# Optimization experiments

Hardware: AMD Instinct MI355X
Metric: run time of the kernel (lower is better)

## Reference

```python
import jax, jax.numpy as jnp
import numpy as np

FP4_E2M1_VALUES = [0.0, 0.0625, 8.0, 1.0, 2.0, 3.0, 4.0, 6.0,
                   -0.0, -0.0625, -8.0, -1.0, -2.0, -3.0, -4.0, -6.0]

M, N, K = 4096, 4096, 4096


def setup_inputs() -> dict:
    key = jax.random.key(0)
    k1, k2 = jax.random.split(key)
    x = jax.random.normal(k1, (M, K), dtype=jnp.float16)
    # packed uint8 bytes stored as int32 (values in [0,256)); each byte holds
    # two fp4 indices: high nibble = even k, low nibble = odd k
    packed_weight = jax.random.randint(k2, (N, K // 2), 0, 256, dtype=jnp.int32)
    lut = jnp.array(FP4_E2M1_VALUES, dtype=jnp.float16)
    return {"x": x, "packed_weight": packed_weight, "lut": lut}


def reference(x, packed_weight, lut):
    # Dequantize: unpack nibbles along K, LUT lookup -> W [N, K] fp16
    n, kh = packed_weight.shape
    high = (packed_weight >> 4) & 15   # even k positions
    low = packed_weight & 15           # odd k positions
    idx = jnp.stack([high, low], axis=-1).reshape(n, 2 * kh)  # [N, K]
    w = lut[idx]                       # [N, K] fp16
    # GEMM with fp32 accumulation (Triton kernel accumulates in fp32), cast to fp16
    y = jnp.einsum('mk,nk->mn', x, w, preferred_element_type=jnp.float32)
    return y.astype(jnp.float16)
```

## Files before the change

### kernel.cpp

```cpp
#include <hip/hip_runtime.h>
#include <hip/hip_fp16.h>
#include <stdint.h>

#define M_DIM 4096
#define N_DIM 4096
#define K_DIM 4096
#define BM 128
#define BN 128
#define BK 32
#define KW (K_DIM / 2)

typedef _Float16 half8 __attribute__((ext_vector_type(8)));
typedef float f32x4 __attribute__((ext_vector_type(4)));

__device__ __forceinline__ uint32_t pk2(float a, float b) {
  auto h = __builtin_amdgcn_cvt_pkrtz(a, b);
  return __builtin_bit_cast(uint32_t, h);
}

__device__ __forceinline__ uint32_t dq(uint32_t b, uint32_t ph, uint32_t pl) {
#if __has_builtin(__builtin_amdgcn_perm)
  const uint32_t sel = ((b & 0x70u) << 4) | ((b & 0x07u) << 24);
  uint32_t v = __builtin_amdgcn_perm(ph, pl, sel);
#else
  const uint64_t pool = ((uint64_t)ph << 32) | pl;
  const uint32_t mh = (uint32_t)(pool >> (((b >> 4) & 7u) * 8)) & 0xFFu;
  const uint32_t ml = (uint32_t)(pool >> ((b & 7u) * 8)) & 0xFFu;
  uint32_t v = (mh << 8) | (ml << 24);
#endif
  const uint32_t sg = ((b & 0x88u) * 0x10000100u) & 0x80008000u;
  return v | sg;
}

__global__ __launch_bounds__(256) void cvt_x_kernel(const float4* __restrict__ xin,
                                                    uint4* __restrict__ xout) {
  const int i = blockIdx.x * 256 + threadIdx.x;
  const float4 v0 = xin[2 * i];
  const float4 v1 = xin[2 * i + 1];
  xout[i] = make_uint4(pk2(v0.x, v0.y), pk2(v0.z, v0.w),
                       pk2(v1.x, v1.y), pk2(v1.z, v1.w));
}

__global__ __launch_bounds__(256, 2) void fp4gemm_kernel(
    const uint8_t* __restrict__ xh,
    const int* __restrict__ pw,
    const float* __restrict__ lutf,
    float* __restrict__ out)
{
  __shared__ uint16_t ldsA[BM * BK];
  __shared__ uint16_t ldsB[BN * BK];

  const int tid  = threadIdx.x;
  const int lane = tid & 63;
  const int wave = tid >> 6;
  const int wm   = wave >> 1;
  const int wn   = wave & 1;
  const int m0 = blockIdx.y * BM;
  const int n0 = blockIdx.x * BN;

  const uint32_t h01 = pk2(lutf[0], lutf[1]);
  const uint32_t h23 = pk2(lutf[2], lutf[3]);
  const uint32_t h45 = pk2(lutf[4], lutf[5]);
  const uint32_t h67 = pk2(lutf[6], lutf[7]);
#if __has_builtin(__builtin_amdgcn_perm)
  const uint32_t pl = __builtin_amdgcn_perm(h23, h01, 0x07050301u);
  const uint32_t ph = __builtin_amdgcn_perm(h67, h45, 0x07050301u);
#else
  const uint32_t pl = ((h01 >> 8) & 0xFFu) | ((h01 >> 24) << 8) |
                      (((h23 >> 8) & 0xFFu) << 16) | ((h23 >> 24) << 24);
  const uint32_t ph = ((h45 >> 8) & 0xFFu) | ((h45 >> 24) << 8) |
                      (((h67 >> 8) & 0xFFu) << 16) | ((h67 >> 24) << 24);
#endif

  f32x4 acc[4][4];
#pragma unroll
  for (int i = 0; i < 4; ++i)
#pragma unroll
    for (int j = 0; j < 4; ++j) acc[i][j] = (f32x4){0.f, 0.f, 0.f, 0.f};

  const int rowB  = tid >> 1;
  const int halfB = tid & 1;

  for (int kt = 0; kt < K_DIM / BK; ++kt) {
    __syncthreads();

#pragma unroll
    for (int s = 0; s < 2; ++s) {
      const int idx = tid + s * 256;
      const int row = idx >> 2;
      const int c16 = idx & 3;
      const uint8_t* gp = xh + ((size_t)(m0 + row) * K_DIM + kt * BK) * 2 + c16 * 16;
      uint8_t* lp = (uint8_t*)ldsA + (size_t)idx * 16;
      __builtin_amdgcn_global_load_lds(
          (const __attribute__((address_space(1))) uint32_t*)gp,
          (__attribute__((address_space(3))) uint32_t*)lp, 16, 0, 0);
    }

    {
      const int* gp = pw + (size_t)(n0 + rowB) * KW + kt * (BK / 2) + halfB * 8;
      const int4 wA = ((const int4*)gp)[0];
      const int4 wB = ((const int4*)gp)[1];
      uint32_t* lb = (uint32_t*)((uint8_t*)ldsB + rowB * 64 + halfB * 32);
      ((uint4*)lb)[0] = make_uint4(dq(wA.x, ph, pl), dq(wA.y, ph, pl),
                                   dq(wA.z, ph, pl), dq(wA.w, ph, pl));
      ((uint4*)lb)[1] = make_uint4(dq(wB.x, ph, pl), dq(wB.y, ph, pl),
                                   dq(wB.z, ph, pl), dq(wB.w, ph, pl));
    }

    __syncthreads();

    half8 af[4], bfr[4];
#pragma unroll
    for (int i = 0; i < 4; ++i) {
      const uint16_t* pa = ldsA + (wm * 64 + i * 16 + (lane & 15)) * BK + (lane >> 4) * 8;
      af[i] = *(const half8*)pa;
    }
#pragma unroll
    for (int j = 0; j < 4; ++j) {
      const uint16_t* pb = ldsB + (wn * 64 + j * 16 + (lane & 15)) * BK + (lane >> 4) * 8;
      bfr[j] = *(const half8*)pb;
    }
#pragma unroll
    for (int i = 0; i < 4; ++i)
#pragma unroll
      for (int j = 0; j < 4; ++j)
        acc[i][j] = __builtin_amdgcn_mfma_f32_16x16x32_f16(af[i], bfr[j], acc[i][j], 0, 0, 0);
  }

  const int mb = m0 + wm * 64 + (lane >> 4) * 4;
  const int nb = n0 + wn * 64 + (lane & 15);
#pragma unroll
  for (int i = 0; i < 4; ++i)
#pragma unroll
    for (int j = 0; j < 4; ++j)
#pragma unroll
      for (int r = 0; r < 4; ++r)
        out[(size_t)(mb + i * 16 + r) * N_DIM + (nb + j * 16)] = acc[i][j][r];
}

extern "C" void kernel_launch(void* const* d_in, const int* in_sizes, int n_in,
                              void* d_out, int out_size, void* d_ws, size_t ws_size,
                              hipStream_t stream) {
  const void* px = nullptr; const void* ppw = nullptr; const void* plut = nullptr;
  for (int i = 0; i < n_in; ++i) {
    const long s = in_sizes[i];
    if (s == (long)M_DIM * K_DIM) px = d_in[i];
    else if (s == (long)N_DIM * KW) ppw = d_in[i];
    else if (s == 16) plut = d_in[i];
  }
  if (!px || !ppw || !plut) { px = d_in[0]; ppw = d_in[1]; plut = d_in[2]; }

  dim3 grid(N_DIM / BN, M_DIM / BM);

  cvt_x_kernel<<<(M_DIM * K_DIM / 8) / 256, 256, 0, stream>>>(
      (const float4*)px, (uint4*)d_ws);
  fp4gemm_kernel<<<grid, dim3(256), 0, stream>>>(
      (const uint8_t*)d_ws, (const int*)ppw, (const float*)plut, (float*)d_out);
}
```

Measured before the change: 311.3 us.

## Dequantize weights directly into MFMA registers and prefetch next tile

Drops the LDS staging buffer for the B operand. Each lane now loads its own packed weight words from global memory and dequantizes them straight into MFMA fragment registers. The next K tile's packed weights are prefetched into registers to hide global latency, which removes the LDS writes, reads and the LDS footprint for B. In exchange, weight loads are duplicated across the two waves that share a column tile (wm=0/1), each wave issues narrower, less coalesced global loads, and register pressure rises.

```diff
diff --git a/kernel.cpp b/kernel.cpp
--- a/kernel.cpp
+++ b/kernel.cpp
@@ -8,6 +8,7 @@
 #define BM 128
 #define BN 128
 #define BK 32
+#define NKT (K_DIM / BK)
 #define KW (K_DIM / 2)
 
 typedef _Float16 half8 __attribute__((ext_vector_type(8)));
@@ -32,6 +33,12 @@
   return v | sg;
 }
 
+__device__ __forceinline__ half8 dq4(const int4 w, uint32_t ph, uint32_t pl) {
+  const uint4 u = make_uint4(dq(w.x, ph, pl), dq(w.y, ph, pl),
+                             dq(w.z, ph, pl), dq(w.w, ph, pl));
+  return __builtin_bit_cast(half8, u);
+}
+
 __global__ __launch_bounds__(256) void cvt_x_kernel(const float4* __restrict__ xin,
                                                     uint4* __restrict__ xout) {
   const int i = blockIdx.x * 256 + threadIdx.x;
@@ -48,7 +55,6 @@
     float* __restrict__ out)
 {
   __shared__ uint16_t ldsA[BM * BK];
-  __shared__ uint16_t ldsB[BN * BK];
 
   const int tid  = threadIdx.x;
   const int lane = tid & 63;
@@ -78,10 +84,16 @@
 #pragma unroll
     for (int j = 0; j < 4; ++j) acc[i][j] = (f32x4){0.f, 0.f, 0.f, 0.f};
 
-  const int rowB  = tid >> 1;
-  const int halfB = tid & 1;
+  const int nr  = n0 + wn * 64 + (lane & 15);
+  const int kq4 = (lane >> 4) * 4;
+  const int* pwb = pw + (size_t)nr * KW + kq4;
 
-  for (int kt = 0; kt < K_DIM / BK; ++kt) {
+  int4 wreg[4];
+#pragma unroll
+  for (int j = 0; j < 4; ++j)
+    wreg[j] = *(const int4*)(pwb + (size_t)j * 16 * KW);
+
+  for (int kt = 0; kt < NKT; ++kt) {
     __syncthreads();
 
 #pragma unroll
@@ -96,29 +108,22 @@
           (__attribute__((address_space(3))) uint32_t*)lp, 16, 0, 0);
     }
 
-    {
-      const int* gp = pw + (size_t)(n0 + rowB) * KW + kt * (BK / 2) + halfB * 8;
-      const int4 wA = ((const int4*)gp)[0];
-      const int4 wB = ((const int4*)gp)[1];
-      uint32_t* lb = (uint32_t*)((uint8_t*)ldsB + rowB * 64 + halfB * 32);
-      ((uint4*)lb)[0] = make_uint4(dq(wA.x, ph, pl), dq(wA.y, ph, pl),
-                                   dq(wA.z, ph, pl), dq(wA.w, ph, pl));
-      ((uint4*)lb)[1] = make_uint4(dq(wB.x, ph, pl), dq(wB.y, ph, pl),
-                                   dq(wB.z, ph, pl), dq(wB.w, ph, pl));
-    }
+    half8 bfr[4];
+#pragma unroll
+    for (int j = 0; j < 4; ++j) bfr[j] = dq4(wreg[j], ph, pl);
 
     __syncthreads();
 
-    half8 af[4], bfr[4];
+    const int ktn = (kt + 1 < NKT) ? kt + 1 : kt;
+#pragma unroll
+    for (int j = 0; j < 4; ++j)
+      wreg[j] = *(const int4*)(pwb + (size_t)j * 16 * KW + ktn * 16);
+
+    half8 af[4];
 #pragma unroll
     for (int i = 0; i < 4; ++i) {
       const uint16_t* pa = ldsA + (wm * 64 + i * 16 + (lane & 15)) * BK + (lane >> 4) * 8;
       af[i] = *(const half8*)pa;
-    }
-#pragma unroll
-    for (int j = 0; j < 4; ++j) {
-      const uint16_t* pb = ldsB + (wn * 64 + j * 16 + (lane & 15)) * BK + (lane >> 4) * 8;
-      bfr[j] = *(const half8*)pb;
     }
 #pragma unroll
     for (int i = 0; i < 4; ++i)
```

Result: slower. 498.5 us (+60.1%).
